# Performance work log

Measured on AMD Instinct MI355X. Metric: run time of the kernel, lower is better.

The kernel has to match this reference:

```python
import jax, jax.numpy as jnp
import numpy as np

N = 50000      # nodes
E = 800000     # edges (avg degree 16)
F_IN = 128     # num_node_features
H = 128        # hidden_channels
B = 64         # graphs in batch
OUT = 1        # output_features


def setup_inputs() -> dict:
    key = jax.random.key(0)
    ks = jax.random.split(key, 12)
    def lin_w(k, fan_in, fan_out):
        return (jax.random.normal(k, (fan_in, fan_out), jnp.float32)
                / np.float32(np.sqrt(fan_in)))
    x = jax.random.normal(ks[0], (N, F_IN), jnp.float32)
    edge_index = jax.random.randint(ks[1], (2, E), 0, N, dtype=jnp.int32)
    batch = jnp.sort(jax.random.randint(ks[2], (N,), 0, B, dtype=jnp.int32))
    return dict(
        x=x, edge_index=edge_index, batch=batch,
        W1=lin_w(ks[3], F_IN, H), b1=jnp.zeros((H,), jnp.float32),
        W2=lin_w(ks[4], H, H),    b2=jnp.zeros((H,), jnp.float32),
        W3=lin_w(ks[5], H, H),    b3=jnp.zeros((H,), jnp.float32),
        fw1=lin_w(ks[6], H, 64),  fb1=jnp.zeros((64,), jnp.float32),
        fw2=lin_w(ks[7], 64, OUT), fb2=jnp.zeros((OUT,), jnp.float32),
    )


def _gcn_conv(x, W, b, src, dst, norm, n_nodes):
    # h = X W; out[i] = sum_{j->i} norm_ij * h[j] + b  (self-loops included in src/dst)
    h = x @ W
    msg = h[src] * norm[:, None]                       # [E+N, H] gather + scale
    return jax.ops.segment_sum(msg, dst, num_segments=n_nodes) + b


def reference(x, edge_index, batch, W1, b1, W2, b2, W3, b3, fw1, fb1, fw2, fb2):
    src, dst = edge_index[0], edge_index[1]
    loop = jnp.arange(N, dtype=src.dtype)
    src = jnp.concatenate([src, loop])                 # add self-loops
    dst = jnp.concatenate([dst, loop])
    deg = jax.ops.segment_sum(jnp.ones_like(dst, jnp.float32), dst,
                              num_segments=N)
    dinv = jax.lax.rsqrt(jnp.maximum(deg, 1.0))        # deg^{-1/2}
    norm = dinv[src] * dinv[dst]                       # symmetric GCN norm per edge

    h = jax.nn.relu(_gcn_conv(x, W1, b1, src, dst, norm, N))
    h = jax.nn.relu(_gcn_conv(h, W2, b2, src, dst, norm, N))
    h = _gcn_conv(h, W3, b3, src, dst, norm, N)

    # global mean pool over graph ids
    sums = jax.ops.segment_sum(h, batch, num_segments=B)
    cnt = jax.ops.segment_sum(jnp.ones((N,), jnp.float32), batch,
                              num_segments=B)
    g = sums / jnp.maximum(cnt, 1.0)[:, None]          # [B, H]

    g = jax.nn.relu(g @ fw1 + fb1)
    return g @ fw2 + fb2                               # [B, OUT]
```

## Files before the change

kernel.cpp:

```cpp
#include <hip/hip_runtime.h>
#include <math.h>

#define N_NODES 50000
#define N_PAD   50048
#define N_EDGES 800000
#define F 128
#define FH 64
#define B_GRAPHS 64
#define SCAN_NB 49
#define N_INT4 12500
#define NBUCKET 196
#define SCAT_CHUNK 4096

using bf16x8 = __attribute__((ext_vector_type(8))) short;
using f32x4  = __attribute__((ext_vector_type(4))) float;
union U4 { uint4 u; bf16x8 v; };


__device__ __forceinline__ unsigned bf16_rne(float a) {
    unsigned u = __float_as_uint(a);
    u += 0x7fffu + ((u >> 16) & 1u);
    return u >> 16;
}

__device__ __forceinline__ unsigned pack_bf16x2(float a, float b) {
    return bf16_rne(a) | (bf16_rne(b) << 16);
}

__device__ __forceinline__ float2 unpack_bf16x2(unsigned p) {
    return make_float2(__uint_as_float(p << 16),
                       __uint_as_float(p & 0xffff0000u));
}

__device__ __forceinline__ void split2(float a, float b, unsigned& hiw, unsigned& low) {
    unsigned ha = bf16_rne(a), hb = bf16_rne(b);
    float ra = a - __uint_as_float(ha << 16);
    float rb = b - __uint_as_float(hb << 16);
    hiw = ha | (hb << 16);
    low = pack_bf16x2(ra, rb);
}


__global__ __launch_bounds__(256) void zero_i32(int* p, int n) {
    int i = blockIdx.x * blockDim.x + threadIdx.x;
    if (i < n) p[i] = 0;
}

__global__ __launch_bounds__(256) void zero_f32(float* p, int n) {
    int i = blockIdx.x * blockDim.x + threadIdx.x;
    if (i < n) p[i] = 0.f;
}


__global__ __launch_bounds__(256) void deg_count(const int* __restrict__ dst,
                                                 int* __restrict__ deg) {
    int e = blockIdx.x * blockDim.x + threadIdx.x;
    if (e < N_EDGES) atomicAdd(&deg[dst[e]], 1);
}

__global__ __launch_bounds__(256) void dinv_kernel(const int* __restrict__ deg,
                                                   float* __restrict__ dinv) {
    int i = blockIdx.x * blockDim.x + threadIdx.x;
    if (i < N_NODES) dinv[i] = rsqrtf((float)(deg[i] + 1));
}


__global__ __launch_bounds__(256) void scan1(const int* __restrict__ deg,
                                             int* __restrict__ off,
                                             int* __restrict__ bsum) {
    __shared__ int wsum[4];
    int b = blockIdx.x, t = threadIdx.x;
    int i4 = b * 256 + t;
    int4 v = make_int4(0, 0, 0, 0);
    if (i4 < N_INT4) v = ((const int4*)deg)[i4];
    int s = v.x + v.y + v.z + v.w;
    int lane = t & 63;
    int incl = s;
#pragma unroll
    for (int d = 1; d < 64; d <<= 1) {
        int u = __shfl_up(incl, d, 64);
        if (lane >= d) incl += u;
    }
    int wave = t >> 6;
    if (lane == 63) wsum[wave] = incl;
    __syncthreads();
    int woff = 0;
#pragma unroll
    for (int w = 0; w < 3; ++w) if (w < wave) woff += wsum[w];
    int texcl = woff + incl - s;
    int4 o;
    o.x = texcl;
    o.y = o.x + v.x;
    o.z = o.y + v.y;
    o.w = o.z + v.z;
    if (i4 < N_INT4) ((int4*)off)[i4] = o;
    if (t == 255) bsum[b] = woff + incl;
}

__global__ __launch_bounds__(64) void scan2(const int* __restrict__ bsum,
                                            int* __restrict__ bexcl,
                                            int* __restrict__ off) {
    int t = threadIdx.x;
    int v = (t < SCAN_NB) ? bsum[t] : 0;
    int incl = v;
#pragma unroll
    for (int d = 1; d < 64; d <<= 1) {
        int u = __shfl_up(incl, d, 64);
        if (t >= d) incl += u;
    }
    if (t < SCAN_NB) bexcl[t] = incl - v;
    if (t == 63) off[N_NODES] = incl;
}

__global__ __launch_bounds__(256) void scan3(int* __restrict__ off,
                                             const int* __restrict__ bexcl) {
    int b = blockIdx.x, t = threadIdx.x;
    int i4 = b * 256 + t;
    if (i4 >= N_INT4) return;
    int add = bexcl[b];
    int4 o = ((int4*)off)[i4];
    o.x += add; o.y += add; o.z += add; o.w += add;
    ((int4*)off)[i4] = o;
}


__global__ __launch_bounds__(256) void init_bcursor(const int* __restrict__ off,
                                                    int* __restrict__ bcursor) {
    int t = threadIdx.x;
    if (t < NBUCKET) bcursor[t] = off[t << 8];
}

__global__ __launch_bounds__(256) void scatter_bucket(const int* __restrict__ src,
                                                      const int* __restrict__ dst,
                                                      int* __restrict__ bcursor,
                                                      unsigned* __restrict__ pairs) {
    __shared__ int lcnt[NBUCKET];
    __shared__ int lbase[NBUCKET];
    int t = threadIdx.x;
    int base = blockIdx.x * SCAT_CHUNK;
    for (int i = t; i < NBUCKET; i += 256) lcnt[i] = 0;
    __syncthreads();
#pragma unroll
    for (int i = 0; i < SCAT_CHUNK / 256; ++i) {
        int idx = base + i * 256 + t;
        if (idx < N_EDGES) atomicAdd(&lcnt[dst[idx] >> 8], 1);
    }
    __syncthreads();
    for (int i = t; i < NBUCKET; i += 256) {
        lbase[i] = atomicAdd(&bcursor[i], lcnt[i]);
        lcnt[i] = 0;
    }
    __syncthreads();
#pragma unroll
    for (int i = 0; i < SCAT_CHUNK / 256; ++i) {
        int idx = base + i * 256 + t;
        if (idx < N_EDGES) {
            int s = src[idx], d = dst[idx];
            int b = d >> 8;
            int pos = lbase[b] + atomicAdd(&lcnt[b], 1);
            pairs[pos] = (unsigned)s | ((unsigned)(d & 255) << 17);
        }
    }
}

__global__ __launch_bounds__(256) void scatter_place(const unsigned* __restrict__ pairs,
                                                     const int* __restrict__ off,
                                                     int* __restrict__ srcs) {
    __shared__ int lcur[256];
    int b = blockIdx.x;
    int n0 = b << 8;
    int t = threadIdx.x;
    int nodeEnd = n0 + 256; if (nodeEnd > N_NODES) nodeEnd = N_NODES;
    if (n0 + t < N_NODES) lcur[t] = off[n0 + t];
    int start = off[n0];
    int end = off[nodeEnd];
    __syncthreads();
    for (int p = start + t; p < end; p += 256) {
        unsigned pr = pairs[p];
        int pos = atomicAdd(&lcur[pr >> 17], 1);
        srcs[pos] = (int)(pr & 0x1FFFFu);
    }
}


__global__ __launch_bounds__(256) void conv_x(const float* __restrict__ x,
                                              unsigned* __restrict__ Xhi,
                                              unsigned* __restrict__ Xlo) {
    int gid = blockIdx.x * 256 + threadIdx.x;
    if (gid >= N_NODES * FH) return;
    float2 v = *(const float2*)&x[(size_t)gid * 2];
    unsigned hw, lw;
    split2(v.x, v.y, hw, lw);
    Xhi[gid] = hw;
    Xlo[gid] = lw;
}

__global__ __launch_bounds__(256) void conv_w(const float* __restrict__ W,
                                              unsigned* __restrict__ Wfh,
                                              unsigned* __restrict__ Wfl) {
    int pos = blockIdx.x * 256 + threadIdx.x;
    if (pos >= 2048) return;
    int lane = pos & 63;
    int kc = (pos >> 6) & 3;
    int nt = pos >> 8;
    int col = nt * 16 + (lane & 15);
    int kg = lane >> 4;
    uint4 hw, lw;
    unsigned* hp = (unsigned*)&hw;
    unsigned* lp = (unsigned*)&lw;
#pragma unroll
    for (int w = 0; w < 4; ++w) {
        int k0 = kc * 32 + kg * 8 + 2 * w;
        float a = W[(size_t)k0 * F + col];
        float b = W[(size_t)(k0 + 1) * F + col];
        split2(a, b, hp[w], lp[w]);
    }
    ((uint4*)Wfh)[pos] = hw;
    ((uint4*)Wfl)[pos] = lw;
}


__global__ __launch_bounds__(256) void gemm_mfma(const unsigned* __restrict__ Xhi,
                                                 const unsigned* __restrict__ Xlo,
                                                 const unsigned* __restrict__ Wfh,
                                                 const unsigned* __restrict__ Wfl,
                                                 const float* __restrict__ dinv,
                                                 unsigned* __restrict__ Hs) {
    __shared__ uint4 lxh[64 * 16];
    __shared__ uint4 lxl[64 * 16];
    const int tid = threadIdx.x;
    const int m0 = blockIdx.x * 64;

#pragma unroll
    for (int i = 0; i < 4; ++i) {
        int idx = i * 256 + tid;
        int row = idx >> 4;
        int g = idx & 15;
        int gs = g ^ (row & 7);
        lxh[row * 16 + gs] = ((const uint4*)Xhi)[(size_t)(m0 + row) * 16 + g];
        lxl[row * 16 + gs] = ((const uint4*)Xlo)[(size_t)(m0 + row) * 16 + g];
    }
    __syncthreads();

    const int wave = tid >> 6, lane = tid & 63;
    const int lr = lane & 15, kg = lane >> 4;
    const int r = wave * 16 + lr;

    f32x4 acc[8];
#pragma unroll
    for (int nt = 0; nt < 8; ++nt) acc[nt] = (f32x4){0.f, 0.f, 0.f, 0.f};

#pragma unroll
    for (int kc = 0; kc < 4; ++kc) {
        int gs = (kc * 4 + kg) ^ (r & 7);
        U4 ah, al;
        ah.u = lxh[r * 16 + gs];
        al.u = lxl[r * 16 + gs];
#pragma unroll
        for (int nt = 0; nt < 8; ++nt) {
            U4 bh, bl;
            bh.u = ((const uint4*)Wfh)[(nt * 4 + kc) * 64 + lane];
            bl.u = ((const uint4*)Wfl)[(nt * 4 + kc) * 64 + lane];
            acc[nt] = __builtin_amdgcn_mfma_f32_16x16x32_bf16(ah.v, bh.v, acc[nt], 0, 0, 0);
            acc[nt] = __builtin_amdgcn_mfma_f32_16x16x32_bf16(ah.v, bl.v, acc[nt], 0, 0, 0);
            acc[nt] = __builtin_amdgcn_mfma_f32_16x16x32_bf16(al.v, bh.v, acc[nt], 0, 0, 0);
        }
    }

#pragma unroll
    for (int rr = 0; rr < 4; ++rr) {
        int row = m0 + wave * 16 + 4 * kg + rr;
        bool ok = row < N_NODES;
        float s = ok ? dinv[row] : 0.f;
#pragma unroll
        for (int nt = 0; nt < 8; ++nt) {
            float v = acc[nt][rr] * s;
            float pv = __shfl_xor(v, 1, 64);
            if (((lane & 1) == 0) && ok) {
                Hs[(size_t)row * FH + ((nt * 16 + lr) >> 1)] = pack_bf16x2(v, pv);
            }
        }
    }
}


__device__ __forceinline__ float2 edge_sum(const unsigned* __restrict__ Hs,
                                           const int* __restrict__ off,
                                           const int* __restrict__ srcs,
                                           int node, int lane) {
    float2 acc = unpack_bf16x2(Hs[(size_t)node * FH + lane]);
    int e0 = off[node], e1 = off[node + 1];
    int e = e0;
    for (; e + 15 < e1; e += 16) {
        int si[16];
#pragma unroll
        for (int j = 0; j < 16; ++j) si[j] = srcs[e + j];
        unsigned p[16];
#pragma unroll
        for (int j = 0; j < 16; ++j) p[j] = Hs[(size_t)si[j] * FH + lane];
        float sx = 0.f, sy = 0.f;
#pragma unroll
        for (int j = 0; j < 16; ++j) {
            float2 v = unpack_bf16x2(p[j]);
            sx += v.x;
            sy += v.y;
        }
        acc.x += sx;
        acc.y += sy;
    }
    for (; e + 3 < e1; e += 4) {
        int si[4];
#pragma unroll
        for (int j = 0; j < 4; ++j) si[j] = srcs[e + j];
        unsigned p[4];
#pragma unroll
        for (int j = 0; j < 4; ++j) p[j] = Hs[(size_t)si[j] * FH + lane];
        float2 t0 = unpack_bf16x2(p[0]), t1 = unpack_bf16x2(p[1]);
        float2 t2 = unpack_bf16x2(p[2]), t3 = unpack_bf16x2(p[3]);
        acc.x += (t0.x + t1.x) + (t2.x + t3.x);
        acc.y += (t0.y + t1.y) + (t2.y + t3.y);
    }
    for (; e < e1; ++e) {
        float2 v = unpack_bf16x2(Hs[(size_t)srcs[e] * FH + lane]);
        acc.x += v.x;
        acc.y += v.y;
    }
    return acc;
}


__global__ __launch_bounds__(256) void aggregate_bf16(const unsigned* __restrict__ Hs,
                                                      const int* __restrict__ off,
                                                      const int* __restrict__ srcs,
                                                      const float* __restrict__ dinv,
                                                      const float* __restrict__ bias,
                                                      unsigned* __restrict__ Xhi,
                                                      unsigned* __restrict__ Xlo) {
    int node = blockIdx.x * 4 + (threadIdx.x >> 6);
    if (node >= N_NODES) return;
    int lane = threadIdx.x & 63;
    float2 acc = edge_sum(Hs, off, srcs, node, lane);
    float d = dinv[node];
    float o0 = fmaxf(fmaf(d, acc.x, bias[2 * lane]), 0.f);
    float o1 = fmaxf(fmaf(d, acc.y, bias[2 * lane + 1]), 0.f);
    unsigned hw, lw;
    split2(o0, o1, hw, lw);
    Xhi[(size_t)node * FH + lane] = hw;
    Xlo[(size_t)node * FH + lane] = lw;
}


__global__ __launch_bounds__(256) void aggregate_pool(const unsigned* __restrict__ Hs,
                                                      const int* __restrict__ off,
                                                      const int* __restrict__ srcs,
                                                      const float* __restrict__ dinv,
                                                      const float* __restrict__ bias,
                                                      const int* __restrict__ batch,
                                                      float* __restrict__ psums) {
    int wg = (blockIdx.x * 256 + threadIdx.x) >> 6;
    int lane = threadIdx.x & 63;
    int n0 = wg * 8;
    if (n0 >= N_NODES) return;
    int n1 = n0 + 8;
    if (n1 > N_NODES) n1 = N_NODES;

    float bx = bias[2 * lane], by = bias[2 * lane + 1];
    float2 racc = make_float2(0.f, 0.f);
    int cur = batch[n0];
    for (int node = n0; node < n1; ++node) {
        float2 acc = edge_sum(Hs, off, srcs, node, lane);
        float d = dinv[node];
        float o0 = fmaf(d, acc.x, bx);
        float o1 = fmaf(d, acc.y, by);
        int b = batch[node];
        if (b != cur) {
            atomicAdd(&psums[cur * F + 2 * lane], racc.x);
            atomicAdd(&psums[cur * F + 2 * lane + 1], racc.y);
            racc = make_float2(0.f, 0.f);
            cur = b;
        }
        racc.x += o0;
        racc.y += o1;
    }
    atomicAdd(&psums[cur * F + 2 * lane], racc.x);
    atomicAdd(&psums[cur * F + 2 * lane + 1], racc.y);
}


__device__ __forceinline__ int lower_bound_dev(const int* __restrict__ a, int n, int v) {
    int lo = 0, hi = n;
    while (lo < hi) {
        int m = (lo + hi) >> 1;
        if (a[m] < v) lo = m + 1; else hi = m;
    }
    return lo;
}

__global__ __launch_bounds__(128) void pool_finalize(const float* __restrict__ psums,
                                                     const int* __restrict__ batch,
                                                     float* __restrict__ g) {
    int b = blockIdx.x;
    int f = threadIdx.x;
    int lo = lower_bound_dev(batch, N_NODES, b);
    int hi = lower_bound_dev(batch, N_NODES, b + 1);
    float cnt = (float)(hi - lo);
    g[b * F + f] = psums[b * F + f] / fmaxf(cnt, 1.0f);
}


__global__ __launch_bounds__(64) void head_kernel(const float* __restrict__ g,
                                                  const float* __restrict__ fw1,
                                                  const float* __restrict__ fb1,
                                                  const float* __restrict__ fw2,
                                                  const float* __restrict__ fb2,
                                                  float* __restrict__ out) {
    int b = blockIdx.x;
    int j = threadIdx.x;
    float h = fb1[j];
    for (int k = 0; k < F; ++k)
        h = fmaf(g[b * F + k], fw1[k * 64 + j], h);
    h = fmaxf(h, 0.f) * fw2[j];
#pragma unroll
    for (int w = 32; w >= 1; w >>= 1) h += __shfl_xor(h, w, 64);
    if (j == 0) out[b] = h + fb2[0];
}


extern "C" void kernel_launch(void* const* d_in, const int* in_sizes, int n_in,
                              void* d_out, int out_size, void* d_ws, size_t ws_size,
                              hipStream_t stream) {
    const float* x    = (const float*)d_in[0];
    const int* eidx   = (const int*)d_in[1];
    const int* batch  = (const int*)d_in[2];
    const float* W1   = (const float*)d_in[3];
    const float* b1   = (const float*)d_in[4];
    const float* W2   = (const float*)d_in[5];
    const float* b2   = (const float*)d_in[6];
    const float* W3   = (const float*)d_in[7];
    const float* b3   = (const float*)d_in[8];
    const float* fw1  = (const float*)d_in[9];
    const float* fb1  = (const float*)d_in[10];
    const float* fw2  = (const float*)d_in[11];
    const float* fb2  = (const float*)d_in[12];
    float* out        = (float*)d_out;

    const int* src = eidx;
    const int* dst = eidx + N_EDGES;

    char* ws = (char*)d_ws;
    size_t p = 0;
    auto alloc = [&](size_t bytes) -> void* {
        void* r = ws + p;
        p = (p + bytes + 255) & ~(size_t)255;
        return r;
    };
    int*      deg    = (int*)     alloc((size_t)N_NODES * 4);
    float*    dinv   = (float*)   alloc((size_t)N_NODES * 4);
    int*      off    = (int*)     alloc((size_t)(N_NODES + 4) * 4);
    int*      srcs   = (int*)     alloc((size_t)N_EDGES * 4);
    int*      bsum   = (int*)     alloc((size_t)SCAN_NB * 4);
    int*      bexcl  = (int*)     alloc((size_t)SCAN_NB * 4);
    int*      bcursor= (int*)     alloc((size_t)NBUCKET * 4);
    unsigned* XpkHi  = (unsigned*)alloc((size_t)N_PAD * FH * 4);
    unsigned* XpkLo  = (unsigned*)alloc((size_t)N_PAD * FH * 4);
    unsigned* HsPk   = (unsigned*)alloc((size_t)N_PAD * FH * 4);
    unsigned* Wf     = (unsigned*)alloc((size_t)6 * 2048 * 16);
    float*    psums  = (float*)   alloc((size_t)B_GRAPHS * F * 4);
    float*    gpool  = (float*)   alloc((size_t)B_GRAPHS * F * 4);
    (void)ws_size;

    unsigned* pairs = HsPk;

    unsigned* Wf1h = Wf + 0 * 8192;
    unsigned* Wf1l = Wf + 1 * 8192;
    unsigned* Wf2h = Wf + 2 * 8192;
    unsigned* Wf2l = Wf + 3 * 8192;
    unsigned* Wf3h = Wf + 4 * 8192;
    unsigned* Wf3l = Wf + 5 * 8192;

    const int TB = 256;
    const int nblk_N = (N_NODES + TB - 1) / TB;
    const int nblk_E = (N_EDGES + TB - 1) / TB;
    const int gemm_blocks = N_PAD / 64;
    const int agg_blocks = (N_NODES + 3) / 4;
    const int aggp_blocks = (6250 + 3) / 4 + 1;
    const int convx_blocks = (N_NODES * FH + TB - 1) / TB;
    const int scatA_blocks = (N_EDGES + SCAT_CHUNK - 1) / SCAT_CHUNK;

    zero_i32<<<nblk_N, TB, 0, stream>>>(deg, N_NODES);
    deg_count<<<nblk_E, TB, 0, stream>>>(dst, deg);
    dinv_kernel<<<nblk_N, TB, 0, stream>>>(deg, dinv);

    scan1<<<SCAN_NB, 256, 0, stream>>>(deg, off, bsum);
    scan2<<<1, 64, 0, stream>>>(bsum, bexcl, off);
    scan3<<<SCAN_NB, 256, 0, stream>>>(off, bexcl);
    init_bcursor<<<1, 256, 0, stream>>>(off, bcursor);
    scatter_bucket<<<scatA_blocks, 256, 0, stream>>>(src, dst, bcursor, pairs);
    scatter_place<<<NBUCKET, 256, 0, stream>>>(pairs, off, srcs);

    conv_x<<<convx_blocks, TB, 0, stream>>>(x, XpkHi, XpkLo);
    conv_w<<<8, TB, 0, stream>>>(W1, Wf1h, Wf1l);
    conv_w<<<8, TB, 0, stream>>>(W2, Wf2h, Wf2l);
    conv_w<<<8, TB, 0, stream>>>(W3, Wf3h, Wf3l);
    zero_f32<<<(B_GRAPHS * F + TB - 1) / TB, TB, 0, stream>>>(psums, B_GRAPHS * F);

    gemm_mfma<<<gemm_blocks, 256, 0, stream>>>(XpkHi, XpkLo, Wf1h, Wf1l, dinv, HsPk);
    aggregate_bf16<<<agg_blocks, 256, 0, stream>>>(HsPk, off, srcs, dinv, b1, XpkHi, XpkLo);

    gemm_mfma<<<gemm_blocks, 256, 0, stream>>>(XpkHi, XpkLo, Wf2h, Wf2l, dinv, HsPk);
    aggregate_bf16<<<agg_blocks, 256, 0, stream>>>(HsPk, off, srcs, dinv, b2, XpkHi, XpkLo);

    gemm_mfma<<<gemm_blocks, 256, 0, stream>>>(XpkHi, XpkLo, Wf3h, Wf3l, dinv, HsPk);
    aggregate_pool<<<aggp_blocks, 256, 0, stream>>>(HsPk, off, srcs, dinv, b3, batch, psums);

    pool_finalize<<<B_GRAPHS, 128, 0, stream>>>(psums, batch, gpool);
    head_kernel<<<B_GRAPHS, 64, 0, stream>>>(gpool, fw1, fb1, fw2, fb2, out);
}
```

Measured before the change: 348.2 us.

## Split feature rows into column quarters to improve gather cache locality

Stores the bf16 hidden features and split inputs in a column-quartered layout: four planes of 16 words per node. Aggregation kernels now launch one grid slice per quarter, and each wave handles one node with four sub-groups striding over its edges, then combines them with cross-lane shuffles. The aim is to shrink the working set per pass so the random neighbour gathers hit in L2/MALL more often, and to spread the edge loop across lanes. The cost is reading the edge list four times, extra shuffle reductions, and idle lanes in the epilogue, where only sub 0 writes.

Measured after the change: 492.2 us. 41.4% more time.

```diff
diff --git a/kernel.cpp b/kernel.cpp
--- a/kernel.cpp
+++ b/kernel.cpp
@@ -11,6 +11,8 @@
 #define N_INT4 12500
 #define NBUCKET 196
 #define SCAT_CHUNK 4096
+#define AGG_NB 12500
+#define AGGP_NB 1563
 
 using bf16x8 = __attribute__((ext_vector_type(8))) short;
 using f32x4  = __attribute__((ext_vector_type(4))) float;
@@ -191,8 +193,10 @@
     float2 v = *(const float2*)&x[(size_t)gid * 2];
     unsigned hw, lw;
     split2(v.x, v.y, hw, lw);
-    Xhi[gid] = hw;
-    Xlo[gid] = lw;
+    int node = gid >> 6, word = gid & 63;
+    size_t oidx = ((size_t)(word >> 4) * N_PAD + node) * 16 + (word & 15);
+    Xhi[oidx] = hw;
+    Xlo[oidx] = lw;
 }
 
 __global__ __launch_bounds__(256) void conv_w(const float* __restrict__ W,
@@ -237,8 +241,9 @@
         int row = idx >> 4;
         int g = idx & 15;
         int gs = g ^ (row & 7);
-        lxh[row * 16 + gs] = ((const uint4*)Xhi)[(size_t)(m0 + row) * 16 + g];
-        lxl[row * 16 + gs] = ((const uint4*)Xlo)[(size_t)(m0 + row) * 16 + g];
+        size_t qbase = (size_t)(g >> 2) * N_PAD * 4;
+        lxh[row * 16 + gs] = ((const uint4*)Xhi)[qbase + (size_t)(m0 + row) * 4 + (g & 3)];
+        lxl[row * 16 + gs] = ((const uint4*)Xlo)[qbase + (size_t)(m0 + row) * 4 + (g & 3)];
     }
     __syncthreads();
 
@@ -277,113 +282,118 @@
             float v = acc[nt][rr] * s;
             float pv = __shfl_xor(v, 1, 64);
             if (((lane & 1) == 0) && ok) {
-                Hs[(size_t)row * FH + ((nt * 16 + lr) >> 1)] = pack_bf16x2(v, pv);
+                int word = (nt * 16 + lr) >> 1;
+                Hs[((size_t)(word >> 4) * N_PAD + row) * 16 + (word & 15)] = pack_bf16x2(v, pv);
             }
         }
     }
 }
 
 
-__device__ __forceinline__ float2 edge_sum(const unsigned* __restrict__ Hs,
-                                           const int* __restrict__ off,
-                                           const int* __restrict__ srcs,
-                                           int node, int lane) {
-    float2 acc = unpack_bf16x2(Hs[(size_t)node * FH + lane]);
+__device__ __forceinline__ float2 edge_sum_q(const unsigned* __restrict__ HsQ,
+                                             const int* __restrict__ off,
+                                             const int* __restrict__ srcs,
+                                             int node, int sub, int w) {
+    float2 acc = make_float2(0.f, 0.f);
     int e0 = off[node], e1 = off[node + 1];
-    int e = e0;
-    for (; e + 15 < e1; e += 16) {
-        int si[16];
-#pragma unroll
-        for (int j = 0; j < 16; ++j) si[j] = srcs[e + j];
-        unsigned p[16];
-#pragma unroll
-        for (int j = 0; j < 16; ++j) p[j] = Hs[(size_t)si[j] * FH + lane];
-        float sx = 0.f, sy = 0.f;
-#pragma unroll
-        for (int j = 0; j < 16; ++j) {
-            float2 v = unpack_bf16x2(p[j]);
-            sx += v.x;
-            sy += v.y;
-        }
-        acc.x += sx;
-        acc.y += sy;
-    }
-    for (; e + 3 < e1; e += 4) {
-        int si[4];
-#pragma unroll
-        for (int j = 0; j < 4; ++j) si[j] = srcs[e + j];
-        unsigned p[4];
-#pragma unroll
-        for (int j = 0; j < 4; ++j) p[j] = Hs[(size_t)si[j] * FH + lane];
-        float2 t0 = unpack_bf16x2(p[0]), t1 = unpack_bf16x2(p[1]);
-        float2 t2 = unpack_bf16x2(p[2]), t3 = unpack_bf16x2(p[3]);
+    int e = e0 + sub;
+    for (; e + 12 < e1; e += 16) {
+        int s0 = srcs[e], s1 = srcs[e + 4], s2 = srcs[e + 8], s3 = srcs[e + 12];
+        unsigned p0 = HsQ[(size_t)s0 * 16 + w];
+        unsigned p1 = HsQ[(size_t)s1 * 16 + w];
+        unsigned p2 = HsQ[(size_t)s2 * 16 + w];
+        unsigned p3 = HsQ[(size_t)s3 * 16 + w];
+        float2 t0 = unpack_bf16x2(p0), t1 = unpack_bf16x2(p1);
+        float2 t2 = unpack_bf16x2(p2), t3 = unpack_bf16x2(p3);
         acc.x += (t0.x + t1.x) + (t2.x + t3.x);
         acc.y += (t0.y + t1.y) + (t2.y + t3.y);
     }
-    for (; e < e1; ++e) {
-        float2 v = unpack_bf16x2(Hs[(size_t)srcs[e] * FH + lane]);
-        acc.x += v.x;
-        acc.y += v.y;
-    }
+    for (; e < e1; e += 4) {
+        float2 t = unpack_bf16x2(HsQ[(size_t)srcs[e] * 16 + w]);
+        acc.x += t.x;
+        acc.y += t.y;
+    }
+    acc.x += __shfl_xor(acc.x, 16, 64);
+    acc.y += __shfl_xor(acc.y, 16, 64);
+    acc.x += __shfl_xor(acc.x, 32, 64);
+    acc.y += __shfl_xor(acc.y, 32, 64);
+    float2 self = unpack_bf16x2(HsQ[(size_t)node * 16 + w]);
+    acc.x += self.x;
+    acc.y += self.y;
     return acc;
 }
 
 
-__global__ __launch_bounds__(256) void aggregate_bf16(const unsigned* __restrict__ Hs,
-                                                      const int* __restrict__ off,
-                                                      const int* __restrict__ srcs,
-                                                      const float* __restrict__ dinv,
-                                                      const float* __restrict__ bias,
-                                                      unsigned* __restrict__ Xhi,
-                                                      unsigned* __restrict__ Xlo) {
-    int node = blockIdx.x * 4 + (threadIdx.x >> 6);
-    if (node >= N_NODES) return;
+__global__ __launch_bounds__(256) void aggregate_q(const unsigned* __restrict__ HsAll,
+                                                   const int* __restrict__ off,
+                                                   const int* __restrict__ srcs,
+                                                   const float* __restrict__ dinv,
+                                                   const float* __restrict__ bias,
+                                                   unsigned* __restrict__ XhiAll,
+                                                   unsigned* __restrict__ XloAll) {
+    int q = blockIdx.x / AGG_NB;
+    int nb = blockIdx.x % AGG_NB;
+    int node = nb * 4 + (threadIdx.x >> 6);
     int lane = threadIdx.x & 63;
-    float2 acc = edge_sum(Hs, off, srcs, node, lane);
-    float d = dinv[node];
-    float o0 = fmaxf(fmaf(d, acc.x, bias[2 * lane]), 0.f);
-    float o1 = fmaxf(fmaf(d, acc.y, bias[2 * lane + 1]), 0.f);
-    unsigned hw, lw;
-    split2(o0, o1, hw, lw);
-    Xhi[(size_t)node * FH + lane] = hw;
-    Xlo[(size_t)node * FH + lane] = lw;
-}
-
-
-__global__ __launch_bounds__(256) void aggregate_pool(const unsigned* __restrict__ Hs,
-                                                      const int* __restrict__ off,
-                                                      const int* __restrict__ srcs,
-                                                      const float* __restrict__ dinv,
-                                                      const float* __restrict__ bias,
-                                                      const int* __restrict__ batch,
-                                                      float* __restrict__ psums) {
-    int wg = (blockIdx.x * 256 + threadIdx.x) >> 6;
+    int sub = lane >> 4, w = lane & 15;
+    const unsigned* HsQ = HsAll + (size_t)q * N_PAD * 16;
+    float2 acc = edge_sum_q(HsQ, off, srcs, node, sub, w);
+    if (sub == 0) {
+        float d = dinv[node];
+        int f = (q * 16 + w) * 2;
+        float o0 = fmaxf(fmaf(d, acc.x, bias[f]), 0.f);
+        float o1 = fmaxf(fmaf(d, acc.y, bias[f + 1]), 0.f);
+        unsigned hw, lw;
+        split2(o0, o1, hw, lw);
+        size_t oidx = ((size_t)q * N_PAD + node) * 16 + w;
+        XhiAll[oidx] = hw;
+        XloAll[oidx] = lw;
+    }
+}
+
+
+__global__ __launch_bounds__(256) void aggregate_pool_q(const unsigned* __restrict__ HsAll,
+                                                        const int* __restrict__ off,
+                                                        const int* __restrict__ srcs,
+                                                        const float* __restrict__ dinv,
+                                                        const float* __restrict__ bias,
+                                                        const int* __restrict__ batch,
+                                                        float* __restrict__ psums) {
+    int q = blockIdx.x / AGGP_NB;
+    int nb = blockIdx.x % AGGP_NB;
+    int wg = nb * 4 + (threadIdx.x >> 6);
     int lane = threadIdx.x & 63;
+    int sub = lane >> 4, w = lane & 15;
     int n0 = wg * 8;
     if (n0 >= N_NODES) return;
     int n1 = n0 + 8;
     if (n1 > N_NODES) n1 = N_NODES;
-
-    float bx = bias[2 * lane], by = bias[2 * lane + 1];
+    const unsigned* HsQ = HsAll + (size_t)q * N_PAD * 16;
+    int f = (q * 16 + w) * 2;
+    float bx = bias[f], by = bias[f + 1];
     float2 racc = make_float2(0.f, 0.f);
     int cur = batch[n0];
     for (int node = n0; node < n1; ++node) {
-        float2 acc = edge_sum(Hs, off, srcs, node, lane);
+        float2 acc = edge_sum_q(HsQ, off, srcs, node, sub, w);
         float d = dinv[node];
         float o0 = fmaf(d, acc.x, bx);
         float o1 = fmaf(d, acc.y, by);
         int b = batch[node];
         if (b != cur) {
-            atomicAdd(&psums[cur * F + 2 * lane], racc.x);
-            atomicAdd(&psums[cur * F + 2 * lane + 1], racc.y);
+            if (sub == 0) {
+                atomicAdd(&psums[cur * F + f], racc.x);
+                atomicAdd(&psums[cur * F + f + 1], racc.y);
+            }
             racc = make_float2(0.f, 0.f);
             cur = b;
         }
         racc.x += o0;
         racc.y += o1;
     }
-    atomicAdd(&psums[cur * F + 2 * lane], racc.x);
-    atomicAdd(&psums[cur * F + 2 * lane + 1], racc.y);
+    if (sub == 0) {
+        atomicAdd(&psums[cur * F + f], racc.x);
+        atomicAdd(&psums[cur * F + f + 1], racc.y);
+    }
 }
 
 
@@ -482,8 +492,8 @@
     const int nblk_N = (N_NODES + TB - 1) / TB;
     const int nblk_E = (N_EDGES + TB - 1) / TB;
     const int gemm_blocks = N_PAD / 64;
-    const int agg_blocks = (N_NODES + 3) / 4;
-    const int aggp_blocks = (6250 + 3) / 4 + 1;
+    const int agg_blocks = 4 * AGG_NB;
+    const int aggp_blocks = 4 * AGGP_NB;
     const int convx_blocks = (N_NODES * FH + TB - 1) / TB;
     const int scatA_blocks = (N_EDGES + SCAT_CHUNK - 1) / SCAT_CHUNK;
 
@@ -505,13 +515,13 @@
     zero_f32<<<(B_GRAPHS * F + TB - 1) / TB, TB, 0, stream>>>(psums, B_GRAPHS * F);
 
     gemm_mfma<<<gemm_blocks, 256, 0, stream>>>(XpkHi, XpkLo, Wf1h, Wf1l, dinv, HsPk);
-    aggregate_bf16<<<agg_blocks, 256, 0, stream>>>(HsPk, off, srcs, dinv, b1, XpkHi, XpkLo);
+    aggregate_q<<<agg_blocks, 256, 0, stream>>>(HsPk, off, srcs, dinv, b1, XpkHi, XpkLo);
 
     gemm_mfma<<<gemm_blocks, 256, 0, stream>>>(XpkHi, XpkLo, Wf2h, Wf2l, dinv, HsPk);
-    aggregate_bf16<<<agg_blocks, 256, 0, stream>>>(HsPk, off, srcs, dinv, b2, XpkHi, XpkLo);
+    aggregate_q<<<agg_blocks, 256, 0, stream>>>(HsPk, off, srcs, dinv, b2, XpkHi, XpkLo);
 
     gemm_mfma<<<gemm_blocks, 256, 0, stream>>>(XpkHi, XpkLo, Wf3h, Wf3l, dinv, HsPk);
-    aggregate_pool<<<aggp_blocks, 256, 0, stream>>>(HsPk, off, srcs, dinv, b3, batch, psums);
+    aggregate_pool_q<<<aggp_blocks, 256, 0, stream>>>(HsPk, off, srcs, dinv, b3, batch, psums);
 
     pool_finalize<<<B_GRAPHS, 128, 0, stream>>>(psums, batch, gpool);
     head_kernel<<<B_GRAPHS, 64, 0, stream>>>(gpool, fw1, fb1, fw2, fb2, out);
```
